# Optimization experiments

Hardware: AMD Instinct MI355X
Metric: run time of the kernel (lower is better)

## Reference

```python
import jax, jax.numpy as jnp
import numpy as np


def setup_inputs() -> dict:
    key = jax.random.key(0)
    ks = jax.random.split(key, 7)
    N, D, C, SY, SX = 512, 256, 128, 12, 12
    return {
        "f_t": jax.random.normal(ks[0], (N, D), dtype=jnp.float32),
        "fmap_t": jax.random.normal(ks[1], (N, SY, SX, C), dtype=jnp.float32),
        "fmap_tp1": jax.random.normal(ks[2], (N, SY, SX, C), dtype=jnp.float32),
        "W1": jax.random.normal(ks[3], (C, D), dtype=jnp.float32) * 0.05,
        "b1": jax.random.normal(ks[4], (C,), dtype=jnp.float32) * 0.05,
        "W2": jax.random.normal(ks[5], (C, C), dtype=jnp.float32) * 0.05,
        "b2": jax.random.normal(ks[6], (C,), dtype=jnp.float32) * 0.05,
    }


def _ce_diag(logits):
    # logits: [L, N, N]; labels are arange(N) per location.
    lse = jax.nn.logsumexp(logits, axis=-1)           # [L, N]
    diag = jnp.diagonal(logits, axis1=1, axis2=2)     # [L, N]
    # mean over batch per location, then mean over locations == sum/L in torch code
    return jnp.mean(lse - diag)


def reference(f_t, fmap_t, fmap_tp1, W1, b1, W2, b2):
    N = f_t.shape[0]
    C = fmap_tp1.shape[-1]
    # flatten spatial grid: [L, N, C]
    pos = fmap_tp1.reshape(N, -1, C).transpose(1, 0, 2)
    loc = fmap_t.reshape(N, -1, C).transpose(1, 0, 2)

    # loss1: global-local. classifier1(f_t) is loop-invariant -> computed once.
    preds1 = f_t @ W1.T + b1                          # [N, C]
    logits1 = jnp.einsum('nc,lmc->lnm', preds1, pos)  # [L, N, N]
    loss1 = _ce_diag(logits1)

    # loss2: local-local, per-location linear fused as batched einsum.
    preds2 = jnp.einsum('lnc,dc->lnd', loc, W2) + b2  # [L, N, C]
    logits2 = jnp.einsum('lnc,lmc->lnm', preds2, pos) # [L, N, N]
    loss2 = _ce_diag(logits2)

    return loss1 + loss2
```

## Files before the change

### kernel.cpp

```cpp
#include <hip/hip_runtime.h>
#include <hip/hip_bf16.h>
#include <math.h>

#define LC 18432
#define LOG2E 1.4426950408889634f

typedef short bf16x8 __attribute__((ext_vector_type(8)));
typedef float f32x4 __attribute__((ext_vector_type(4)));

#define MFMA16 __builtin_amdgcn_mfma_f32_16x16x32_bf16

__device__ __forceinline__ float fast_exp2(float x) {
#if __has_builtin(__builtin_amdgcn_exp2f)
  return __builtin_amdgcn_exp2f(x);
#else
  return exp2f(x);
#endif
}
__device__ __forceinline__ float fast_log2(float x) {
#if __has_builtin(__builtin_amdgcn_logf)
  return __builtin_amdgcn_logf(x);
#else
  return log2f(x);
#endif
}

__device__ __forceinline__ ushort f2bf(float x) {
  __hip_bfloat16 h = __float2bfloat16(x);
  return __builtin_bit_cast(ushort, h);
}

__device__ __forceinline__ int swb(int row, int x) {
  return (row << 8) + (x ^ ((row & 15) << 4));
}
__device__ __forceinline__ int swb9(int row, int x) {
  return (row << 9) + (x ^ ((row & 15) << 4));
}

typedef const __attribute__((address_space(1))) unsigned int g_u32;
typedef __attribute__((address_space(3))) unsigned int l_u32;
__device__ __forceinline__ void gl_lds16(const ushort* g, ushort* l) {
  __builtin_amdgcn_global_load_lds((g_u32*)g, (l_u32*)l, 16, 0, 0);
}

__global__ __launch_bounds__(256) void prep_kernel(
    const float* __restrict__ f_t, const float* __restrict__ fmap_t,
    const float* __restrict__ fmap_tp1, const float* __restrict__ W1,
    const float* __restrict__ b1, const float* __restrict__ W2,
    const float* __restrict__ b2, ushort* __restrict__ p1img,
    ushort* __restrict__ p2img, ushort* __restrict__ posimg) {
  __shared__ __align__(16) ushort s_lds[32768];
  const int bid = blockIdx.x, t = threadIdx.x;
  const int wave = t >> 6, lane = t & 63, lo = lane & 15, hi = lane >> 4;

  if (bid < 16) {
    const int rb = bid >> 1, dh = bid & 1;
    ushort* sF = s_lds;
    ushort* sW = s_lds + 16384;
#pragma unroll
    for (int k = 0; k < 16; ++k) {
      int idx = t + k * 256;
      int row = idx >> 6, c4 = (idx & 63) << 2;
      float4 v = *(const float4*)(f_t + (size_t)(rb * 64 + row) * 256 + c4);
      ushort4 h = {f2bf(v.x), f2bf(v.y), f2bf(v.z), f2bf(v.w)};
      *(ushort4*)((char*)sF + swb9(row, c4 << 1)) = h;
    }
#pragma unroll
    for (int k = 0; k < 16; ++k) {
      int idx = t + k * 256;
      int row = idx >> 6, c4 = (idx & 63) << 2;
      float4 v = *(const float4*)(W1 + (size_t)(dh * 64 + row) * 256 + c4);
      ushort4 h = {f2bf(v.x), f2bf(v.y), f2bf(v.z), f2bf(v.w)};
      *(ushort4*)((char*)sW + swb9(row, c4 << 1)) = h;
    }
    __syncthreads();
    const int wn = (wave & 1) * 32, wd = (wave >> 1) * 32;
    f32x4 acc[2][2] = {};
#pragma unroll
    for (int s = 0; s < 8; ++s) {
      int x = s * 64 + hi * 16;
      bf16x8 a0 = *(const bf16x8*)((const char*)sF + swb9(wn + lo, x));
      bf16x8 a1 = *(const bf16x8*)((const char*)sF + swb9(wn + 16 + lo, x));
#pragma unroll
      for (int j = 0; j < 2; ++j) {
        bf16x8 b = *(const bf16x8*)((const char*)sW + swb9(wd + j * 16 + lo, x));
        acc[0][j] = MFMA16(a0, b, acc[0][j], 0, 0, 0);
        acc[1][j] = MFMA16(a1, b, acc[1][j], 0, 0, 0);
      }
    }
    ushort* tile = p1img + (size_t)rb * 8192;
#pragma unroll
    for (int j = 0; j < 2; ++j) {
      int d = dh * 64 + wd + j * 16 + lo;
      float bb = b1[d];
#pragma unroll
      for (int i2 = 0; i2 < 2; ++i2)
#pragma unroll
        for (int e = 0; e < 4; ++e) {
          int r = wn + i2 * 16 + hi * 4 + e;
          *(ushort*)((char*)tile + (r << 8) + ((2 * d) ^ ((r & 15) << 4))) =
              f2bf((acc[i2][j][e] + bb) * LOG2E);
        }
    }
  } else if (bid < 1168) {
    const int ba = bid - 16;
    const int l = ba >> 3, rb = ba & 7;
    ushort* sL = s_lds;
    ushort* sW = s_lds + 8192;
#pragma unroll
    for (int k = 0; k < 8; ++k) {
      int idx = t + k * 256;
      int row = idx >> 5, c4 = (idx & 31) << 2;
      float4 v = *(const float4*)(fmap_t + (size_t)(rb * 64 + row) * LC + l * 128 + c4);
      ushort4 h = {f2bf(v.x), f2bf(v.y), f2bf(v.z), f2bf(v.w)};
      *(ushort4*)((char*)sL + swb(row, c4 << 1)) = h;
    }
#pragma unroll
    for (int k = 0; k < 16; ++k) {
      int idx = t + k * 256;
      int row = idx >> 5, c4 = (idx & 31) << 2;
      float4 v = *(const float4*)(W2 + (size_t)row * 128 + c4);
      ushort4 h = {f2bf(v.x), f2bf(v.y), f2bf(v.z), f2bf(v.w)};
      *(ushort4*)((char*)sW + swb(row, c4 << 1)) = h;
    }
    __syncthreads();
    const int wn = (wave & 1) * 32, wd = (wave >> 1) * 64;
    f32x4 acc[2][4] = {};
#pragma unroll
    for (int s = 0; s < 4; ++s) {
      int x = s * 64 + hi * 16;
      bf16x8 a0 = *(const bf16x8*)((const char*)sL + swb(wn + lo, x));
      bf16x8 a1 = *(const bf16x8*)((const char*)sL + swb(wn + 16 + lo, x));
#pragma unroll
      for (int j = 0; j < 4; ++j) {
        bf16x8 b = *(const bf16x8*)((const char*)sW + swb(wd + j * 16 + lo, x));
        acc[0][j] = MFMA16(a0, b, acc[0][j], 0, 0, 0);
        acc[1][j] = MFMA16(a1, b, acc[1][j], 0, 0, 0);
      }
    }
    ushort* tile = p2img + (size_t)ba * 8192;
#pragma unroll
    for (int j = 0; j < 4; ++j) {
      int d = wd + j * 16 + lo;
      float bb = b2[d];
#pragma unroll
      for (int i2 = 0; i2 < 2; ++i2)
#pragma unroll
        for (int e = 0; e < 4; ++e) {
          int r = wn + i2 * 16 + hi * 4 + e;
          *(ushort*)((char*)tile + (r << 8) + ((2 * d) ^ ((r & 15) << 4))) =
              f2bf((acc[i2][j][e] + bb) * LOG2E);
        }
    }
  } else {
    const int bb = bid - 1168;
    const int l = bb >> 3, mt = bb & 7;
    ushort* tile = posimg + (size_t)bb * 8192;
#pragma unroll
    for (int k = 0; k < 8; ++k) {
      int idx = t + k * 256;
      int row = idx >> 5, c4 = (idx & 31) << 2;
      float4 v = *(const float4*)(fmap_tp1 + (size_t)(mt * 64 + row) * LC + l * 128 + c4);
      ushort4 h = {f2bf(v.x), f2bf(v.y), f2bf(v.z), f2bf(v.w)};
      *(ushort4*)((char*)tile + swb(row, c4 << 1)) = h;
    }
  }
}

__global__ __launch_bounds__(512) void stdim_main(
    const ushort* __restrict__ p1img, const ushort* __restrict__ p2img,
    const ushort* __restrict__ posimg, float* __restrict__ out) {
  __shared__ __align__(16) ushort sB[2][8192];
  __shared__ float s_rows[2][64][2];
  __shared__ float s_diag[2][64];
  __shared__ float s_red[8];

  const int bid = blockIdx.x;
  const int work = (bid & 7) * 144 + (bid >> 3);
  const int l = work >> 3, rb = work & 7;
  const int t = threadIdx.x;
  const int wave = t >> 6, lane = t & 63, lo = lane & 15, hi = lane >> 4;
  const int ty_ = wave >> 2, wr = (wave >> 1) & 1, wc = wave & 1;

  const ushort* ptile = posimg + (size_t)(l * 8) * 8192;

  {
    const ushort* src = ptile + wave * 1024 + lane * 8;
    ushort* dst = (ushort*)sB[0] + wave * 1024;
    gl_lds16(src, dst);
    gl_lds16(src + 512, dst + 512);
  }

  const ushort* aimg = ty_ ? (p2img + (size_t)(l * 8 + rb) * 8192)
                           : (p1img + (size_t)rb * 8192);
  bf16x8 af[2][4];
#pragma unroll
  for (int rt = 0; rt < 2; ++rt)
#pragma unroll
    for (int s = 0; s < 4; ++s)
      af[rt][s] = *(const bf16x8*)((const char*)aimg +
                                   swb(wr * 32 + rt * 16 + lo, s * 64 + hi * 16));

  float sm0[4] = {0.f, 0.f, 0.f, 0.f}, sm1[4] = {0.f, 0.f, 0.f, 0.f};
  __syncthreads();

  for (int mt = 0; mt < 8; ++mt) {
    const int cur = mt & 1;
    if (mt < 7) {
      const ushort* src = ptile + (size_t)(mt + 1) * 8192 + wave * 1024 + lane * 8;
      ushort* dst = (ushort*)sB[cur ^ 1] + wave * 1024;
      gl_lds16(src, dst);
      gl_lds16(src + 512, dst + 512);
    }
    f32x4 a00 = {}, a01 = {}, a10 = {}, a11 = {};
#pragma unroll
    for (int s = 0; s < 4; ++s) {
      int x = s * 64 + hi * 16;
      bf16x8 b0 = *(const bf16x8*)((const char*)sB[cur] + swb(wc * 32 + lo, x));
      bf16x8 b1 = *(const bf16x8*)((const char*)sB[cur] + swb(wc * 32 + 16 + lo, x));
      a00 = MFMA16(af[0][s], b0, a00, 0, 0, 0);
      a01 = MFMA16(af[0][s], b1, a01, 0, 0, 0);
      a10 = MFMA16(af[1][s], b0, a10, 0, 0, 0);
      a11 = MFMA16(af[1][s], b1, a11, 0, 0, 0);
    }
#pragma unroll
    for (int i = 0; i < 4; ++i) {
      sm0[i] += fast_exp2(a00[i]) + fast_exp2(a01[i]);
      sm1[i] += fast_exp2(a10[i]) + fast_exp2(a11[i]);
    }
    if (mt == rb && wc == wr) {
#pragma unroll
      for (int i = 0; i < 4; ++i) {
        if (lo == hi * 4 + i) {
          s_diag[ty_][wr * 32 + hi * 4 + i] = a00[i];
          s_diag[ty_][wr * 32 + 16 + hi * 4 + i] = a11[i];
        }
      }
    }
    __syncthreads();
  }

#pragma unroll
  for (int i = 0; i < 4; ++i) {
    float v0 = sm0[i], v1 = sm1[i];
#pragma unroll
    for (int st = 1; st <= 8; st <<= 1) {
      v0 += __shfl_xor(v0, st);
      v1 += __shfl_xor(v1, st);
    }
    sm0[i] = v0;
    sm1[i] = v1;
  }
  if (lo == 0) {
#pragma unroll
    for (int i = 0; i < 4; ++i) {
      s_rows[ty_][wr * 32 + hi * 4 + i][wc] = sm0[i];
      s_rows[ty_][wr * 32 + 16 + hi * 4 + i][wc] = sm1[i];
    }
  }
  __syncthreads();

  float part = 0.f;
  if (t < 128) {
    int ty = t >> 6, r = t & 63;
    float tot = s_rows[ty][r][0] + s_rows[ty][r][1];
    part = fast_log2(tot) - s_diag[ty][r];
  }
#pragma unroll
  for (int st = 1; st <= 32; st <<= 1) part += __shfl_xor(part, st);
  if (lane == 0) s_red[wave] = part;
  __syncthreads();
  if (t == 0) {
    float s = 0.f;
#pragma unroll
    for (int w = 0; w < 8; ++w) s += s_red[w];
    atomicAdd(out, s * (0.6931471805599453f / 73728.0f));
  }
}

extern "C" void kernel_launch(void* const* d_in, const int* in_sizes, int n_in,
                              void* d_out, int out_size, void* d_ws, size_t ws_size,
                              hipStream_t stream) {
  const float* f_t      = (const float*)d_in[0];
  const float* fmap_t   = (const float*)d_in[1];
  const float* fmap_tp1 = (const float*)d_in[2];
  const float* W1       = (const float*)d_in[3];
  const float* b1       = (const float*)d_in[4];
  const float* W2       = (const float*)d_in[5];
  const float* b2       = (const float*)d_in[6];
  float* out = (float*)d_out;

  ushort* p1img  = (ushort*)d_ws;
  ushort* p2img  = p1img + 8 * 8192;
  ushort* posimg = p2img + 1152 * 8192;

  hipMemsetAsync(d_out, 0, out_size * sizeof(float), stream);
  prep_kernel<<<2320, 256, 0, stream>>>(f_t, fmap_t, fmap_tp1, W1, b1, W2, b2,
                                        p1img, p2img, posimg);
  stdim_main<<<1152, 512, 0, stream>>>(p1img, p2img, posimg, out);
}
```

Baseline: 166.8 us.

## Deepen pos-tile LDS prefetch to four buffers with vmcnt-gated barriers

The double-buffered LDS staging of the positive-feature tiles becomes a four-slot ring that prefetches three tiles ahead. Each iteration now waits with explicit s_waitcnt vmcnt counts and a raw s_barrier, replacing the end-of-iteration __syncthreads. The aim is to hide global-to-LDS latency behind the MFMA and exp work and to drop one barrier per tile. In exchange, LDS use per block doubles to about 64KB, which may limit how many blocks fit on a CU, and correctness now depends on the hand-counted vmcnt values.

```diff
diff --git a/kernel.cpp b/kernel.cpp
--- a/kernel.cpp
+++ b/kernel.cpp
@@ -9,6 +9,7 @@
 typedef float f32x4 __attribute__((ext_vector_type(4)));
 
 #define MFMA16 __builtin_amdgcn_mfma_f32_16x16x32_bf16
+#define WAITVM(N) asm volatile("s_waitcnt vmcnt(" #N ")" ::: "memory")
 
 __device__ __forceinline__ float fast_exp2(float x) {
 #if __has_builtin(__builtin_amdgcn_exp2f)
@@ -170,7 +171,7 @@
 __global__ __launch_bounds__(512) void stdim_main(
     const ushort* __restrict__ p1img, const ushort* __restrict__ p2img,
     const ushort* __restrict__ posimg, float* __restrict__ out) {
-  __shared__ __align__(16) ushort sB[2][8192];
+  __shared__ __align__(16) ushort sB[4][8192];
   __shared__ float s_rows[2][64][2];
   __shared__ float s_diag[2][64];
   __shared__ float s_red[8];
@@ -183,13 +184,8 @@
   const int ty_ = wave >> 2, wr = (wave >> 1) & 1, wc = wave & 1;
 
   const ushort* ptile = posimg + (size_t)(l * 8) * 8192;
-
-  {
-    const ushort* src = ptile + wave * 1024 + lane * 8;
-    ushort* dst = (ushort*)sB[0] + wave * 1024;
-    gl_lds16(src, dst);
-    gl_lds16(src + 512, dst + 512);
-  }
+  const ushort* gsrc = ptile + wave * 1024 + lane * 8;
+  ushort* const ldst0 = (ushort*)sB[0] + wave * 1024;
 
   const ushort* aimg = ty_ ? (p2img + (size_t)(l * 8 + rb) * 8192)
                            : (p1img + (size_t)rb * 8192);
@@ -200,24 +196,37 @@
     for (int s = 0; s < 4; ++s)
       af[rt][s] = *(const bf16x8*)((const char*)aimg +
                                    swb(wr * 32 + rt * 16 + lo, s * 64 + hi * 16));
+#pragma unroll
+  for (int pt = 0; pt < 3; ++pt) {
+    gl_lds16(gsrc + (size_t)pt * 8192, ldst0 + pt * 8192);
+    gl_lds16(gsrc + (size_t)pt * 8192 + 512, ldst0 + pt * 8192 + 512);
+  }
+  WAITVM(0);
 
   float sm0[4] = {0.f, 0.f, 0.f, 0.f}, sm1[4] = {0.f, 0.f, 0.f, 0.f};
-  __syncthreads();
-
+
+#pragma unroll
   for (int mt = 0; mt < 8; ++mt) {
-    const int cur = mt & 1;
-    if (mt < 7) {
-      const ushort* src = ptile + (size_t)(mt + 1) * 8192 + wave * 1024 + lane * 8;
-      ushort* dst = (ushort*)sB[cur ^ 1] + wave * 1024;
+    if (mt < 6) WAITVM(4);
+    else if (mt == 6) WAITVM(2);
+    else WAITVM(0);
+    __builtin_amdgcn_s_barrier();
+    __builtin_amdgcn_sched_barrier(0);
+
+    if (mt <= 4) {
+      const ushort* src = gsrc + (size_t)(mt + 3) * 8192;
+      ushort* dst = ldst0 + ((mt + 3) & 3) * 8192;
       gl_lds16(src, dst);
       gl_lds16(src + 512, dst + 512);
     }
+
+    const ushort* cur = sB[mt & 3];
     f32x4 a00 = {}, a01 = {}, a10 = {}, a11 = {};
 #pragma unroll
     for (int s = 0; s < 4; ++s) {
       int x = s * 64 + hi * 16;
-      bf16x8 b0 = *(const bf16x8*)((const char*)sB[cur] + swb(wc * 32 + lo, x));
-      bf16x8 b1 = *(const bf16x8*)((const char*)sB[cur] + swb(wc * 32 + 16 + lo, x));
+      bf16x8 b0 = *(const bf16x8*)((const char*)cur + swb(wc * 32 + lo, x));
+      bf16x8 b1 = *(const bf16x8*)((const char*)cur + swb(wc * 32 + 16 + lo, x));
       a00 = MFMA16(af[0][s], b0, a00, 0, 0, 0);
       a01 = MFMA16(af[0][s], b1, a01, 0, 0, 0);
       a10 = MFMA16(af[1][s], b0, a10, 0, 0, 0);
@@ -237,7 +246,6 @@
         }
       }
     }
-    __syncthreads();
   }
 
 #pragma unroll
```

Measured after the change: 163.8 us. No clear change (-1.8%).

## Fuse preds2 and pos conversion into main kernel, drop workspace images

Applied to the files above, without the earlier changes.

Removes the bf16 workspace images for preds2 and pos. The main kernel now computes preds2 per block from fmap_t and W2 in LDS, and converts fmap_tp1 tiles from fp32 in registers with a two-ahead prefetch into double-buffered LDS. A small separate kernel computes preds1 and zeroes the output, replacing the memset. This cuts the intermediate global write and re-read traffic and one launch. In exchange each pos tile is read and converted by all 8 row-block blocks of a location, and the main kernel uses more registers and LDS.

```diff
diff --git a/kernel.cpp b/kernel.cpp
--- a/kernel.cpp
+++ b/kernel.cpp
@@ -37,140 +37,85 @@
   return (row << 9) + (x ^ ((row & 15) << 4));
 }
 
-typedef const __attribute__((address_space(1))) unsigned int g_u32;
-typedef __attribute__((address_space(3))) unsigned int l_u32;
-__device__ __forceinline__ void gl_lds16(const ushort* g, ushort* l) {
-  __builtin_amdgcn_global_load_lds((g_u32*)g, (l_u32*)l, 16, 0, 0);
-}
-
-__global__ __launch_bounds__(256) void prep_kernel(
-    const float* __restrict__ f_t, const float* __restrict__ fmap_t,
-    const float* __restrict__ fmap_tp1, const float* __restrict__ W1,
-    const float* __restrict__ b1, const float* __restrict__ W2,
-    const float* __restrict__ b2, ushort* __restrict__ p1img,
-    ushort* __restrict__ p2img, ushort* __restrict__ posimg) {
-  __shared__ __align__(16) ushort s_lds[32768];
-  const int bid = blockIdx.x, t = threadIdx.x;
+__global__ __launch_bounds__(256) void preds1_k(
+    const float* __restrict__ f_t, const float* __restrict__ W1,
+    const float* __restrict__ b1, ushort* __restrict__ p1img,
+    float* __restrict__ out) {
+  if (blockIdx.x == 0 && threadIdx.x == 0) *out = 0.f;
+  __shared__ __align__(16) ushort sF[32 * 256];
+  __shared__ __align__(16) ushort sW[64 * 256];
+  const int rc = blockIdx.x >> 1, dh = blockIdx.x & 1;
+  const int t = threadIdx.x;
   const int wave = t >> 6, lane = t & 63, lo = lane & 15, hi = lane >> 4;
-
-  if (bid < 16) {
-    const int rb = bid >> 1, dh = bid & 1;
-    ushort* sF = s_lds;
-    ushort* sW = s_lds + 16384;
-#pragma unroll
-    for (int k = 0; k < 16; ++k) {
-      int idx = t + k * 256;
-      int row = idx >> 6, c4 = (idx & 63) << 2;
-      float4 v = *(const float4*)(f_t + (size_t)(rb * 64 + row) * 256 + c4);
-      ushort4 h = {f2bf(v.x), f2bf(v.y), f2bf(v.z), f2bf(v.w)};
-      *(ushort4*)((char*)sF + swb9(row, c4 << 1)) = h;
-    }
-#pragma unroll
-    for (int k = 0; k < 16; ++k) {
-      int idx = t + k * 256;
-      int row = idx >> 6, c4 = (idx & 63) << 2;
-      float4 v = *(const float4*)(W1 + (size_t)(dh * 64 + row) * 256 + c4);
-      ushort4 h = {f2bf(v.x), f2bf(v.y), f2bf(v.z), f2bf(v.w)};
-      *(ushort4*)((char*)sW + swb9(row, c4 << 1)) = h;
-    }
-    __syncthreads();
-    const int wn = (wave & 1) * 32, wd = (wave >> 1) * 32;
-    f32x4 acc[2][2] = {};
-#pragma unroll
-    for (int s = 0; s < 8; ++s) {
-      int x = s * 64 + hi * 16;
-      bf16x8 a0 = *(const bf16x8*)((const char*)sF + swb9(wn + lo, x));
-      bf16x8 a1 = *(const bf16x8*)((const char*)sF + swb9(wn + 16 + lo, x));
-#pragma unroll
-      for (int j = 0; j < 2; ++j) {
-        bf16x8 b = *(const bf16x8*)((const char*)sW + swb9(wd + j * 16 + lo, x));
-        acc[0][j] = MFMA16(a0, b, acc[0][j], 0, 0, 0);
-        acc[1][j] = MFMA16(a1, b, acc[1][j], 0, 0, 0);
-      }
-    }
-    ushort* tile = p1img + (size_t)rb * 8192;
+#pragma unroll
+  for (int k = 0; k < 8; ++k) {
+    int idx = t + k * 256;
+    int row = idx >> 6, c4 = (idx & 63) << 2;
+    float4 v = *(const float4*)(f_t + (size_t)(rc * 32 + row) * 256 + c4);
+    ushort4 h = {f2bf(v.x), f2bf(v.y), f2bf(v.z), f2bf(v.w)};
+    *(ushort4*)((char*)sF + swb9(row, c4 << 1)) = h;
+  }
+#pragma unroll
+  for (int k = 0; k < 16; ++k) {
+    int idx = t + k * 256;
+    int row = idx >> 6, c4 = (idx & 63) << 2;
+    float4 v = *(const float4*)(W1 + (size_t)(dh * 64 + row) * 256 + c4);
+    ushort4 h = {f2bf(v.x), f2bf(v.y), f2bf(v.z), f2bf(v.w)};
+    *(ushort4*)((char*)sW + swb9(row, c4 << 1)) = h;
+  }
+  __syncthreads();
+  const int rn = (wave & 1) * 16, wd = (wave >> 1) * 32;
+  f32x4 acc[2] = {};
+#pragma unroll
+  for (int s = 0; s < 8; ++s) {
+    int x = s * 64 + hi * 16;
+    bf16x8 a = *(const bf16x8*)((const char*)sF + swb9(rn + lo, x));
 #pragma unroll
     for (int j = 0; j < 2; ++j) {
-      int d = dh * 64 + wd + j * 16 + lo;
-      float bb = b1[d];
-#pragma unroll
-      for (int i2 = 0; i2 < 2; ++i2)
-#pragma unroll
-        for (int e = 0; e < 4; ++e) {
-          int r = wn + i2 * 16 + hi * 4 + e;
-          *(ushort*)((char*)tile + (r << 8) + ((2 * d) ^ ((r & 15) << 4))) =
-              f2bf((acc[i2][j][e] + bb) * LOG2E);
-        }
-    }
-  } else if (bid < 1168) {
-    const int ba = bid - 16;
-    const int l = ba >> 3, rb = ba & 7;
-    ushort* sL = s_lds;
-    ushort* sW = s_lds + 8192;
-#pragma unroll
-    for (int k = 0; k < 8; ++k) {
-      int idx = t + k * 256;
-      int row = idx >> 5, c4 = (idx & 31) << 2;
-      float4 v = *(const float4*)(fmap_t + (size_t)(rb * 64 + row) * LC + l * 128 + c4);
-      ushort4 h = {f2bf(v.x), f2bf(v.y), f2bf(v.z), f2bf(v.w)};
-      *(ushort4*)((char*)sL + swb(row, c4 << 1)) = h;
-    }
-#pragma unroll
-    for (int k = 0; k < 16; ++k) {
-      int idx = t + k * 256;
-      int row = idx >> 5, c4 = (idx & 31) << 2;
-      float4 v = *(const float4*)(W2 + (size_t)row * 128 + c4);
-      ushort4 h = {f2bf(v.x), f2bf(v.y), f2bf(v.z), f2bf(v.w)};
-      *(ushort4*)((char*)sW + swb(row, c4 << 1)) = h;
-    }
-    __syncthreads();
-    const int wn = (wave & 1) * 32, wd = (wave >> 1) * 64;
-    f32x4 acc[2][4] = {};
-#pragma unroll
-    for (int s = 0; s < 4; ++s) {
-      int x = s * 64 + hi * 16;
-      bf16x8 a0 = *(const bf16x8*)((const char*)sL + swb(wn + lo, x));
-      bf16x8 a1 = *(const bf16x8*)((const char*)sL + swb(wn + 16 + lo, x));
-#pragma unroll
-      for (int j = 0; j < 4; ++j) {
-        bf16x8 b = *(const bf16x8*)((const char*)sW + swb(wd + j * 16 + lo, x));
-        acc[0][j] = MFMA16(a0, b, acc[0][j], 0, 0, 0);
-        acc[1][j] = MFMA16(a1, b, acc[1][j], 0, 0, 0);
-      }
-    }
-    ushort* tile = p2img + (size_t)ba * 8192;
-#pragma unroll
-    for (int j = 0; j < 4; ++j) {
-      int d = wd + j * 16 + lo;
-      float bb = b2[d];
-#pragma unroll
-      for (int i2 = 0; i2 < 2; ++i2)
-#pragma unroll
-        for (int e = 0; e < 4; ++e) {
-          int r = wn + i2 * 16 + hi * 4 + e;
-          *(ushort*)((char*)tile + (r << 8) + ((2 * d) ^ ((r & 15) << 4))) =
-              f2bf((acc[i2][j][e] + bb) * LOG2E);
-        }
-    }
-  } else {
-    const int bb = bid - 1168;
-    const int l = bb >> 3, mt = bb & 7;
-    ushort* tile = posimg + (size_t)bb * 8192;
-#pragma unroll
-    for (int k = 0; k < 8; ++k) {
-      int idx = t + k * 256;
-      int row = idx >> 5, c4 = (idx & 31) << 2;
-      float4 v = *(const float4*)(fmap_tp1 + (size_t)(mt * 64 + row) * LC + l * 128 + c4);
-      ushort4 h = {f2bf(v.x), f2bf(v.y), f2bf(v.z), f2bf(v.w)};
-      *(ushort4*)((char*)tile + swb(row, c4 << 1)) = h;
-    }
-  }
-}
-
-__global__ __launch_bounds__(512) void stdim_main(
-    const ushort* __restrict__ p1img, const ushort* __restrict__ p2img,
-    const ushort* __restrict__ posimg, float* __restrict__ out) {
-  __shared__ __align__(16) ushort sB[2][8192];
+      bf16x8 b = *(const bf16x8*)((const char*)sW + swb9(wd + j * 16 + lo, x));
+      acc[j] = MFMA16(a, b, acc[j], 0, 0, 0);
+    }
+  }
+#pragma unroll
+  for (int j = 0; j < 2; ++j) {
+    int d = dh * 64 + wd + j * 16 + lo;
+    float bb = b1[d];
+#pragma unroll
+    for (int e = 0; e < 4; ++e) {
+      int R = rc * 32 + rn + hi * 4 + e;
+      int tile = R >> 6, rin = R & 63;
+      *(ushort*)((char*)p1img + (size_t)tile * 16384 + (rin << 8) +
+                 ((2 * d) ^ ((rin & 15) << 4))) =
+          f2bf((acc[j][e] + bb) * LOG2E);
+    }
+  }
+}
+
+__device__ __forceinline__ void load_tile(float4 pv[4], const float* __restrict__ base,
+                                          int t) {
+#pragma unroll
+  for (int k = 0; k < 4; ++k) {
+    int idx = t + k * 512;
+    int row = idx >> 5, c4 = (idx & 31) << 2;
+    pv[k] = *(const float4*)(base + (size_t)row * LC + c4);
+  }
+}
+__device__ __forceinline__ void write_tile(ushort* dstbuf, const float4 pv[4], int t) {
+#pragma unroll
+  for (int k = 0; k < 4; ++k) {
+    int idx = t + k * 512;
+    int row = idx >> 5, c4 = (idx & 31) << 2;
+    ushort4 h = {f2bf(pv[k].x), f2bf(pv[k].y), f2bf(pv[k].z), f2bf(pv[k].w)};
+    *(ushort4*)((char*)dstbuf + swb(row, c4 << 1)) = h;
+  }
+}
+
+__global__ __launch_bounds__(512) void stdim_fused(
+    const ushort* __restrict__ p1img, const float* __restrict__ fmap_t,
+    const float* __restrict__ fmap_tp1, const float* __restrict__ W2,
+    const float* __restrict__ b2, float* __restrict__ out) {
+  __shared__ __align__(16) ushort sP[8192];
+  __shared__ __align__(16) ushort sPos[16384];
   __shared__ float s_rows[2][64][2];
   __shared__ float s_diag[2][64];
   __shared__ float s_red[8];
@@ -182,42 +127,92 @@
   const int wave = t >> 6, lane = t & 63, lo = lane & 15, hi = lane >> 4;
   const int ty_ = wave >> 2, wr = (wave >> 1) & 1, wc = wave & 1;
 
-  const ushort* ptile = posimg + (size_t)(l * 8) * 8192;
-
-  {
-    const ushort* src = ptile + wave * 1024 + lane * 8;
-    ushort* dst = (ushort*)sB[0] + wave * 1024;
-    gl_lds16(src, dst);
-    gl_lds16(src + 512, dst + 512);
-  }
-
-  const ushort* aimg = ty_ ? (p2img + (size_t)(l * 8 + rb) * 8192)
-                           : (p1img + (size_t)rb * 8192);
+  const float* posbase = fmap_tp1 + l * 128;
+
+#pragma unroll
+  for (int k = 0; k < 4; ++k) {
+    int idx = t + k * 512;
+    int row = idx >> 5, c4 = (idx & 31) << 2;
+    float4 v = *(const float4*)(fmap_t + (size_t)(rb * 64 + row) * LC + l * 128 + c4);
+    ushort4 h = {f2bf(v.x), f2bf(v.y), f2bf(v.z), f2bf(v.w)};
+    *(ushort4*)((char*)sP + swb(row, c4 << 1)) = h;
+  }
+#pragma unroll
+  for (int k = 0; k < 8; ++k) {
+    int idx = t + k * 512;
+    int row = idx >> 5, c4 = (idx & 31) << 2;
+    float4 v = *(const float4*)(W2 + (size_t)row * 128 + c4);
+    ushort4 h = {f2bf(v.x), f2bf(v.y), f2bf(v.z), f2bf(v.w)};
+    *(ushort4*)((char*)sPos + swb(row, c4 << 1)) = h;
+  }
+  const int wn = (wave & 1) * 32, wd = (wave >> 1) * 32;
+  const float b2a = b2[wd + lo], b2b = b2[wd + 16 + lo];
+  float4 pvA[4], pvB[4];
+  load_tile(pvA, posbase, t);
+  load_tile(pvB, posbase + (size_t)64 * LC, t);
+  __syncthreads();
+
+  f32x4 acc2[2][2] = {};
+#pragma unroll
+  for (int s = 0; s < 4; ++s) {
+    int x = s * 64 + hi * 16;
+    bf16x8 a0 = *(const bf16x8*)((const char*)sP + swb(wn + lo, x));
+    bf16x8 a1 = *(const bf16x8*)((const char*)sP + swb(wn + 16 + lo, x));
+#pragma unroll
+    for (int j = 0; j < 2; ++j) {
+      bf16x8 b = *(const bf16x8*)((const char*)sPos + swb(wd + j * 16 + lo, x));
+      acc2[0][j] = MFMA16(a0, b, acc2[0][j], 0, 0, 0);
+      acc2[1][j] = MFMA16(a1, b, acc2[1][j], 0, 0, 0);
+    }
+  }
+  __syncthreads();
+
+#pragma unroll
+  for (int i2 = 0; i2 < 2; ++i2)
+#pragma unroll
+    for (int j = 0; j < 2; ++j)
+#pragma unroll
+      for (int e = 0; e < 4; ++e) {
+        int r = wn + i2 * 16 + hi * 4 + e;
+        int d = wd + j * 16 + lo;
+        *(ushort*)((char*)sP + (r << 8) + ((2 * d) ^ ((r & 15) << 4))) =
+            f2bf((acc2[i2][j][e] + (j ? b2b : b2a)) * LOG2E);
+      }
+  write_tile((ushort*)sPos, pvA, t);
+  write_tile((ushort*)((char*)sPos + 16384), pvB, t);
+  __syncthreads();
+
   bf16x8 af[2][4];
-#pragma unroll
-  for (int rt = 0; rt < 2; ++rt)
-#pragma unroll
-    for (int s = 0; s < 4; ++s)
-      af[rt][s] = *(const bf16x8*)((const char*)aimg +
-                                   swb(wr * 32 + rt * 16 + lo, s * 64 + hi * 16));
+  if (ty_ == 0) {
+    const char* aimg = (const char*)(p1img + (size_t)rb * 8192);
+#pragma unroll
+    for (int rt = 0; rt < 2; ++rt)
+#pragma unroll
+      for (int s = 0; s < 4; ++s)
+        af[rt][s] = *(const bf16x8*)(aimg + swb(wr * 32 + rt * 16 + lo, s * 64 + hi * 16));
+  } else {
+#pragma unroll
+    for (int rt = 0; rt < 2; ++rt)
+#pragma unroll
+      for (int s = 0; s < 4; ++s)
+        af[rt][s] = *(const bf16x8*)((const char*)sP +
+                                     swb(wr * 32 + rt * 16 + lo, s * 64 + hi * 16));
+  }
 
   float sm0[4] = {0.f, 0.f, 0.f, 0.f}, sm1[4] = {0.f, 0.f, 0.f, 0.f};
-  __syncthreads();
-
+
+#pragma unroll
   for (int mt = 0; mt < 8; ++mt) {
-    const int cur = mt & 1;
-    if (mt < 7) {
-      const ushort* src = ptile + (size_t)(mt + 1) * 8192 + wave * 1024 + lane * 8;
-      ushort* dst = (ushort*)sB[cur ^ 1] + wave * 1024;
-      gl_lds16(src, dst);
-      gl_lds16(src + 512, dst + 512);
-    }
+    float4 nv[4];
+    if (mt < 6) load_tile(nv, posbase + (size_t)((mt + 2) * 64) * LC, t);
+
+    const char* cur = (const char*)sPos + (mt & 1) * 16384;
     f32x4 a00 = {}, a01 = {}, a10 = {}, a11 = {};
 #pragma unroll
     for (int s = 0; s < 4; ++s) {
       int x = s * 64 + hi * 16;
-      bf16x8 b0 = *(const bf16x8*)((const char*)sB[cur] + swb(wc * 32 + lo, x));
-      bf16x8 b1 = *(const bf16x8*)((const char*)sB[cur] + swb(wc * 32 + 16 + lo, x));
+      bf16x8 b0 = *(const bf16x8*)(cur + swb(wc * 32 + lo, x));
+      bf16x8 b1 = *(const bf16x8*)(cur + swb(wc * 32 + 16 + lo, x));
       a00 = MFMA16(af[0][s], b0, a00, 0, 0, 0);
       a01 = MFMA16(af[0][s], b1, a01, 0, 0, 0);
       a10 = MFMA16(af[1][s], b0, a10, 0, 0, 0);
@@ -238,6 +233,8 @@
       }
     }
     __syncthreads();
+    if (mt < 6)
+      write_tile((ushort*)((char*)sPos + (mt & 1) * 16384), nv, t);
   }
 
 #pragma unroll
@@ -289,13 +286,8 @@
   const float* W2       = (const float*)d_in[5];
   const float* b2       = (const float*)d_in[6];
   float* out = (float*)d_out;
-
-  ushort* p1img  = (ushort*)d_ws;
-  ushort* p2img  = p1img + 8 * 8192;
-  ushort* posimg = p2img + 1152 * 8192;
-
-  hipMemsetAsync(d_out, 0, out_size * sizeof(float), stream);
-  prep_kernel<<<2320, 256, 0, stream>>>(f_t, fmap_t, fmap_tp1, W1, b1, W2, b2,
-                                        p1img, p2img, posimg);
-  stdim_main<<<1152, 512, 0, stream>>>(p1img, p2img, posimg, out);
-}
+  ushort* p1img = (ushort*)d_ws;
+
+  preds1_k<<<32, 256, 0, stream>>>(f_t, W1, b1, p1img, out);
+  stdim_fused<<<1152, 512, 0, stream>>>(p1img, fmap_t, fmap_tp1, W2, b2, out);
+}
```

Result: faster. 153.7 us (-7.9%).
